# Kernel tuning notes

Measured on AMD Instinct MI355X. Metric: run time of the kernel, lower is better.

The kernel has to match this reference:

```python
import jax, jax.numpy as jnp
import numpy as np

B, N, C, K = 8, 4096, 128, 20  # batch, points-per-cloud, channels (n_cout), knn neighbors
NEG_SLOPE = 0.01  # torch F.leaky_relu default


def setup_inputs() -> dict:
    key = jax.random.key(0)
    ks = jax.random.split(key, 6)
    s = 1.0 / np.sqrt(C).astype(np.float32)
    xyz = jax.random.normal(ks[0], (B, 3, N), jnp.float32)
    points = jax.random.normal(ks[1], (B, C, N), jnp.float32)
    Wc = jax.random.normal(ks[2], (C, C), jnp.float32) * s  # center 1x1 conv weight (out,in)
    bc = jax.random.normal(ks[3], (C,), jnp.float32) * s
    Wg = jax.random.normal(ks[4], (C, C), jnp.float32) * s  # grouped 1x1 conv weight
    bg = jax.random.normal(ks[5], (C,), jnp.float32) * s
    return {"xyz": xyz, "points": points, "Wc": Wc, "bc": bc, "Wg": Wg, "bg": bg}


def reference(xyz, points, Wc, bc, Wg, bg):
    # xyz: [B,3,N], points: [B,C,N]
    k = K
    shortcut = points
    p = jax.nn.leaky_relu(points, NEG_SLOPE)        # [B,C,N]
    pt = jnp.transpose(p, (0, 2, 1))                # [B,N,C]
    xt = jnp.transpose(xyz, (0, 2, 1))              # [B,N,3]

    # pairwise squared distances [B,N,N]
    sq_norm = jnp.sum(xt * xt, axis=-1)             # [B,N]
    sq = sq_norm[:, :, None] - 2.0 * jnp.einsum('bnd,bmd->bnm', xt, xt) + sq_norm[:, None, :]

    # knn: k+1 nearest (incl. self), drop self -> [B,N,k]
    _, idx = jax.lax.top_k(-sq, k + 1)
    idx = idx[:, :, 1:]

    # gather neighbor features: [B,N,k,C]
    grouped = jax.vmap(lambda a, i: a[i])(pt, idx)

    # center 1x1 conv on [B,C,1,N] == per-point linear
    center = jnp.einsum('oc,bcn->bon', Wc, p) + bc[None, :, None]      # [B,C,N]
    # grouped 1x1 conv on [B,C,k,N]
    gout = jnp.einsum('oc,bnkc->bokn', Wg, grouped) + bg[None, :, None, None]  # [B,C,k,N]

    # mean over concat([center(1), grouped(k)], axis=2) then residual
    pooled = (center + jnp.sum(gout, axis=2)) / (k + 1)
    return pooled + shortcut
```

## Files before the change

kernel.cpp:

```cpp
#include <hip/hip_runtime.h>

#define B 8
#define N 4096
#define C 128
#define C2 256
#define KNN 21
#define CAP 22

typedef unsigned long long u64;
typedef unsigned int u32;
typedef unsigned short u16;

typedef __attribute__((ext_vector_type(8))) short bf16x8;
typedef __attribute__((ext_vector_type(4))) float f32x4;

__device__ __forceinline__ float bf2f(u16 u) {
    return __uint_as_float(((u32)u) << 16);
}
__device__ __forceinline__ u16 f2bf(float f) {
    u32 x = __float_as_uint(f);
    return (u16)((x + 0x7FFFu + ((x >> 16) & 1u)) >> 16);
}

__global__ __launch_bounds__(256) void k_transpose_lrelu(
        const float* __restrict__ pts, u16* __restrict__ X,
        const float* __restrict__ xyz, float4* __restrict__ cand) {
    __shared__ u16 tile[32][33];
    int b  = blockIdx.z;
    int c0 = blockIdx.y * 32;
    int n0 = blockIdx.x * 32;
    int tx = threadIdx.x, ty = threadIdx.y;

    if (blockIdx.y == 0 && ty == 0) {
        int n = n0 + tx;
        const float* xz = xyz + (size_t)b * 3 * N;
        float x = xz[n], y = xz[N + n], z = xz[2 * N + n];
        float sn = __fadd_rn(__fadd_rn(__fmul_rn(x, x), __fmul_rn(y, y)),
                             __fmul_rn(z, z));
        cand[(size_t)b * N + n] = make_float4(x, y, z, sn);
    }

    const float* src = pts + (size_t)b * C * N;
    #pragma unroll
    for (int i = 0; i < 32; i += 8) {
        float v = src[(size_t)(c0 + ty + i) * N + n0 + tx];
        if (v < 0.f) v = __fmul_rn(v, 0.01f);
        tile[ty + i][tx] = f2bf(v);
    }
    __syncthreads();
    u16* dst = X + (size_t)b * N * C2;
    #pragma unroll
    for (int i = 0; i < 32; i += 8) {
        dst[(size_t)(n0 + ty + i) * C2 + (c0 + tx)] = tile[tx][ty + i];
    }
}

__global__ __launch_bounds__(256) void k_knn_gather(
        const float4* __restrict__ cand, u16* __restrict__ X) {
    __shared__ __align__(16) char lds[52224];
    float4* stg  = (float4*)lds;
    u32*    kbuf = (u32*)(lds + 18432);
    u16*    ibuf = (u16*)(lds + 18432 + 22528);
    u64*    mg   = (u64*)lds;
    __shared__ u16 win[64 * KNN];

    int tid = threadIdx.x;
    int w = tid >> 6, l = tid & 63;
    int b = blockIdx.y;
    int n0 = blockIdx.x * 64;
    int nq = n0 + l;

    const float4* candb = cand + (size_t)b * N;
    float4 cq = candb[nq];
    float qx = cq.x, qy = cq.y, qz = cq.z, snq = cq.w;

    u32 key[KNN], idx[KNN];
    #pragma unroll
    for (int i = 0; i < KNN; ++i) { key[i] = 0xFFFFFFFFu; idx[i] = 0u; }
    int cnt = 0;
    u32 thr = 0xFFFFFFFFu;

    auto compact = [&]() {
        #pragma unroll 1
        for (int i = 0; i < CAP; ++i) {
            if (__ballot(i < cnt) == 0ull) break;
            u32 kv = kbuf[i * 256 + tid];
            u32 iv = ibuf[i * 256 + tid];
            bool ins = (i < cnt) && (kv < key[20]);
            if (__ballot(ins) != 0ull) {
                key[20] = ins ? kv : key[20];
                idx[20] = ins ? iv : idx[20];
                #pragma unroll
                for (int t = 19; t >= 0; --t) {
                    bool sw = key[t] > key[t + 1];
                    u32 ka = sw ? key[t + 1] : key[t];
                    u32 kz = sw ? key[t] : key[t + 1];
                    u32 ia = sw ? idx[t + 1] : idx[t];
                    u32 iz = sw ? idx[t] : idx[t + 1];
                    key[t] = ka; key[t + 1] = kz;
                    idx[t] = ia; idx[t + 1] = iz;
                }
            }
        }
        cnt = 0;
        thr = key[20];
    };

    float4* mystg = stg + w * 288;
    int wl = l + (l >> 3);

    for (int sc = 0; sc < 4; ++sc) {
        int m0 = w * 1024 + sc * 256;
        float4 v0 = candb[m0 + l];
        float4 v1 = candb[m0 + l + 64];
        float4 v2 = candb[m0 + l + 128];
        float4 v3 = candb[m0 + l + 192];
        mystg[wl]       = v0;
        mystg[wl + 72]  = v1;
        mystg[wl + 144] = v2;
        mystg[wl + 216] = v3;
        asm volatile("s_waitcnt lgkmcnt(0)" ::: "memory");
        for (int cc = 0; cc < 256; cc += 8) {
            int base = cc + (cc >> 3);
            #pragma unroll
            for (int j = 0; j < 8; ++j) {
                float4 cp = mystg[base + j];
                int m = m0 + cc + j;
                float dot = __fadd_rn(__fadd_rn(__fmul_rn(qx, cp.x),
                                                __fmul_rn(qy, cp.y)),
                                      __fmul_rn(qz, cp.z));
                float sq = __fadd_rn(__fsub_rn(snq, __fadd_rn(dot, dot)), cp.w);
                u32 bits = __float_as_uint(sq);
                u32 kb = bits ^ (0x80000000u | (u32)(((int)bits) >> 31));
                kbuf[cnt * 256 + tid] = kb;
                ibuf[cnt * 256 + tid] = (u16)m;
                cnt += (kb < thr);
            }
            if (__ballot(cnt >= 15) != 0ull) compact();
        }
    }
    compact();

    __syncthreads();
    #pragma unroll
    for (int j = 0; j < KNN; ++j)
        mg[(w * 64 + l) * KNN + j] = ((u64)key[j] << 32) | (u64)idx[j];
    __syncthreads();

    if (w == 0) {
        int p0 = 0, p1 = 0, p2 = 0, p3 = 0;
        for (int j = 0; j < KNN; ++j) {
            u64 c0 = mg[(0 * 64 + l) * KNN + p0];
            u64 c1 = mg[(1 * 64 + l) * KNN + p1];
            u64 c2 = mg[(2 * 64 + l) * KNN + p2];
            u64 c3 = mg[(3 * 64 + l) * KNN + p3];
            u64 m01 = c0 < c1 ? c0 : c1; int s01 = c0 < c1 ? 0 : 1;
            u64 m23 = c2 < c3 ? c2 : c3; int s23 = c2 < c3 ? 2 : 3;
            u64 mm = m01 < m23 ? m01 : m23;
            int sel = m01 < m23 ? s01 : s23;
            win[l * KNN + j] = (u16)(mm & 0xFFFFu);
            p0 += (sel == 0); p1 += (sel == 1); p2 += (sel == 2); p3 += (sel == 3);
        }
    }
    __syncthreads();

    const u16* Xb = X + (size_t)b * N * C2;
    for (int qq = 0; qq < 16; ++qq) {
        int q = w * 16 + qq;
        float f0 = 0.f, f1 = 0.f;
        #pragma unroll
        for (int j = 1; j < KNN; ++j) {
            int m = win[q * KNN + j];
            u32 u2 = *(const u32*)(Xb + (size_t)m * C2 + 2 * l);
            f0 += bf2f((u16)(u2 & 0xFFFFu));
            f1 += bf2f((u16)(u2 >> 16));
        }
        u16* dst = X + ((size_t)b * N + n0 + q) * C2 + 128 + 2 * l;
        *(u32*)dst = ((u32)f2bf(f1) << 16) | (u32)f2bf(f0);
    }
}

__global__ __launch_bounds__(256) void k_gemm_mfma(
        const u16* __restrict__ X, const float* __restrict__ Wc,
        const float* __restrict__ Wg, const float* __restrict__ pts,
        const float* __restrict__ bc, const float* __restrict__ bg,
        float* __restrict__ out) {
    int lb = (blockIdx.x & 7) * 128 + (blockIdx.x >> 3);
    int wid = lb * 4 + (threadIdx.x >> 6);
    int lane = threadIdx.x & 63;
    int ot = wid & 7;
    int nt = wid >> 3;
    int b  = nt >> 6;
    int n0 = (nt & 63) * 64;

    int l16 = lane & 15, lq = lane >> 4;
    const u16* Xb = X + (size_t)b * N * C2;
    const u16* bptr0 = Xb + (size_t)(n0 + 0 * 16 + l16) * C2 + lq * 8;
    const u16* bptr1 = Xb + (size_t)(n0 + 1 * 16 + l16) * C2 + lq * 8;
    const u16* bptr2 = Xb + (size_t)(n0 + 2 * 16 + l16) * C2 + lq * 8;
    const u16* bptr3 = Xb + (size_t)(n0 + 3 * 16 + l16) * C2 + lq * 8;
    const float* wrowc = Wc + (size_t)(ot * 16 + l16) * 128 + lq * 8;
    const float* wrowg = Wg + (size_t)(ot * 16 + l16) * 128 + lq * 8;

    f32x4 acc0 = {0.f, 0.f, 0.f, 0.f};
    f32x4 acc1 = {0.f, 0.f, 0.f, 0.f};
    f32x4 acc2 = {0.f, 0.f, 0.f, 0.f};
    f32x4 acc3 = {0.f, 0.f, 0.f, 0.f};
    #pragma unroll
    for (int kk = 0; kk < 8; ++kk) {
        const float* ws = (kk < 4) ? (wrowc + kk * 32) : (wrowg + (kk - 4) * 32);
        float4 wa = *(const float4*)ws;
        float4 wb = *(const float4*)(ws + 4);
        bf16x8 a;
        a[0] = (short)f2bf(wa.x); a[1] = (short)f2bf(wa.y);
        a[2] = (short)f2bf(wa.z); a[3] = (short)f2bf(wa.w);
        a[4] = (short)f2bf(wb.x); a[5] = (short)f2bf(wb.y);
        a[6] = (short)f2bf(wb.z); a[7] = (short)f2bf(wb.w);
        bf16x8 b0 = *(const bf16x8*)(bptr0 + kk * 32);
        bf16x8 b1 = *(const bf16x8*)(bptr1 + kk * 32);
        bf16x8 b2 = *(const bf16x8*)(bptr2 + kk * 32);
        bf16x8 b3 = *(const bf16x8*)(bptr3 + kk * 32);
        acc0 = __builtin_amdgcn_mfma_f32_16x16x32_bf16(a, b0, acc0, 0, 0, 0);
        acc1 = __builtin_amdgcn_mfma_f32_16x16x32_bf16(a, b1, acc1, 0, 0, 0);
        acc2 = __builtin_amdgcn_mfma_f32_16x16x32_bf16(a, b2, acc2, 0, 0, 0);
        acc3 = __builtin_amdgcn_mfma_f32_16x16x32_bf16(a, b3, acc3, 0, 0, 0);
    }

    const float inv21 = 1.0f / 21.0f;
    float bias[4];
    #pragma unroll
    for (int r = 0; r < 4; ++r) {
        int o = ot * 16 + lq * 4 + r;
        bias[r] = bc[o] + 20.f * bg[o];
    }
    const float* pb = pts + (size_t)b * C * N;
    float* ob = out + (size_t)b * C * N;
    f32x4 accs[4] = {acc0, acc1, acc2, acc3};
    #pragma unroll
    for (int t = 0; t < 4; ++t) {
        int n = n0 + t * 16 + l16;
        #pragma unroll
        for (int r = 0; r < 4; ++r) {
            int o = ot * 16 + lq * 4 + r;
            ob[(size_t)o * N + n] =
                (accs[t][r] + bias[r]) * inv21 + pb[(size_t)o * N + n];
        }
    }
}

extern "C" void kernel_launch(void* const* d_in, const int* in_sizes, int n_in,
                              void* d_out, int out_size, void* d_ws, size_t ws_size,
                              hipStream_t stream) {
    const float* xyz = (const float*)d_in[0];
    const float* pts = (const float*)d_in[1];
    const float* Wc  = (const float*)d_in[2];
    const float* bc  = (const float*)d_in[3];
    const float* Wg  = (const float*)d_in[4];
    const float* bg  = (const float*)d_in[5];
    float* out = (float*)d_out;

    u16* X = (u16*)d_ws;
    float4* cand = (float4*)((char*)d_ws +
                             (size_t)B * N * C2 * sizeof(u16));

    k_transpose_lrelu<<<dim3(N / 32, C / 32, B), dim3(32, 8), 0, stream>>>(
        pts, X, xyz, cand);
    k_knn_gather<<<dim3(N / 64, B), dim3(256), 0, stream>>>(cand, X);
    k_gemm_mfma<<<dim3(1024), dim3(256), 0, stream>>>(X, Wc, Wg, pts, bc, bg, out);
}
```

Before: 287.4 us.

## Split kNN candidate scan across eight waves per block with two-stage merge

The kNN kernel now runs 512 threads per block, so eight waves each scan 512 candidates instead of four waves scanning 1024. Per-wave partial top-21 lists are merged in two passes, first waves 0-3 into a staging list and then waves 4-7 against it, so the merge buffer fits in LDS. The buffer cap and compaction trigger are lowered to fit the larger thread count, and the padded staging layout is dropped. This shortens the serial scan per query but adds barriers, a second merge pass and more frequent compactions.

```diff
diff --git a/kernel.cpp b/kernel.cpp
--- a/kernel.cpp
+++ b/kernel.cpp
@@ -5,7 +5,7 @@
 #define C 128
 #define C2 256
 #define KNN 21
-#define CAP 22
+#define CAP 15
 
 typedef unsigned long long u64;
 typedef unsigned int u32;
@@ -55,14 +55,15 @@
     }
 }
 
-__global__ __launch_bounds__(256) void k_knn_gather(
+__global__ __launch_bounds__(512) void k_knn_gather(
         const float4* __restrict__ cand, u16* __restrict__ X) {
-    __shared__ __align__(16) char lds[52224];
+    __shared__ __align__(16) char lds[62464];
     float4* stg  = (float4*)lds;
-    u32*    kbuf = (u32*)(lds + 18432);
-    u16*    ibuf = (u16*)(lds + 18432 + 22528);
-    u64*    mg   = (u64*)lds;
-    __shared__ u16 win[64 * KNN];
+    u32*    kbuf = (u32*)(lds + 16384);
+    u16*    ibuf = (u16*)(lds + 47104);
+    u64*    mg4  = (u64*)(lds + 16384);
+    u64*    la   = (u64*)lds;
+    u16*    win  = (u16*)(lds + 10752);
 
     int tid = threadIdx.x;
     int w = tid >> 6, l = tid & 63;
@@ -84,8 +85,8 @@
         #pragma unroll 1
         for (int i = 0; i < CAP; ++i) {
             if (__ballot(i < cnt) == 0ull) break;
-            u32 kv = kbuf[i * 256 + tid];
-            u32 iv = ibuf[i * 256 + tid];
+            u32 kv = kbuf[i * 512 + tid];
+            u32 iv = ibuf[i * 512 + tid];
             bool ins = (i < cnt) && (kv < key[20]);
             if (__ballot(ins) != 0ull) {
                 key[20] = ins ? kv : key[20];
@@ -106,25 +107,19 @@
         thr = key[20];
     };
 
-    float4* mystg = stg + w * 288;
-    int wl = l + (l >> 3);
+    float4* mystg = stg + w * 128;
 
     for (int sc = 0; sc < 4; ++sc) {
-        int m0 = w * 1024 + sc * 256;
+        int m0 = w * 512 + sc * 128;
         float4 v0 = candb[m0 + l];
         float4 v1 = candb[m0 + l + 64];
-        float4 v2 = candb[m0 + l + 128];
-        float4 v3 = candb[m0 + l + 192];
-        mystg[wl]       = v0;
-        mystg[wl + 72]  = v1;
-        mystg[wl + 144] = v2;
-        mystg[wl + 216] = v3;
+        mystg[l]      = v0;
+        mystg[l + 64] = v1;
         asm volatile("s_waitcnt lgkmcnt(0)" ::: "memory");
-        for (int cc = 0; cc < 256; cc += 8) {
-            int base = cc + (cc >> 3);
+        for (int cc = 0; cc < 128; cc += 8) {
             #pragma unroll
             for (int j = 0; j < 8; ++j) {
-                float4 cp = mystg[base + j];
+                float4 cp = mystg[cc + j];
                 int m = m0 + cc + j;
                 float dot = __fadd_rn(__fadd_rn(__fmul_rn(qx, cp.x),
                                                 __fmul_rn(qy, cp.y)),
@@ -132,41 +127,74 @@
                 float sq = __fadd_rn(__fsub_rn(snq, __fadd_rn(dot, dot)), cp.w);
                 u32 bits = __float_as_uint(sq);
                 u32 kb = bits ^ (0x80000000u | (u32)(((int)bits) >> 31));
-                kbuf[cnt * 256 + tid] = kb;
-                ibuf[cnt * 256 + tid] = (u16)m;
+                kbuf[cnt * 512 + tid] = kb;
+                ibuf[cnt * 512 + tid] = (u16)m;
                 cnt += (kb < thr);
             }
-            if (__ballot(cnt >= 15) != 0ull) compact();
+            if (__ballot(cnt >= 8) != 0ull) compact();
         }
     }
     compact();
 
     __syncthreads();
-    #pragma unroll
-    for (int j = 0; j < KNN; ++j)
-        mg[(w * 64 + l) * KNN + j] = ((u64)key[j] << 32) | (u64)idx[j];
+    if (w < 4) {
+        #pragma unroll
+        for (int j = 0; j < KNN; ++j)
+            mg4[(w * 64 + l) * KNN + j] = ((u64)key[j] << 32) | (u64)idx[j];
+    }
     __syncthreads();
 
     if (w == 0) {
         int p0 = 0, p1 = 0, p2 = 0, p3 = 0;
         for (int j = 0; j < KNN; ++j) {
-            u64 c0 = mg[(0 * 64 + l) * KNN + p0];
-            u64 c1 = mg[(1 * 64 + l) * KNN + p1];
-            u64 c2 = mg[(2 * 64 + l) * KNN + p2];
-            u64 c3 = mg[(3 * 64 + l) * KNN + p3];
+            u64 c0 = mg4[(0 * 64 + l) * KNN + p0];
+            u64 c1 = mg4[(1 * 64 + l) * KNN + p1];
+            u64 c2 = mg4[(2 * 64 + l) * KNN + p2];
+            u64 c3 = mg4[(3 * 64 + l) * KNN + p3];
             u64 m01 = c0 < c1 ? c0 : c1; int s01 = c0 < c1 ? 0 : 1;
             u64 m23 = c2 < c3 ? c2 : c3; int s23 = c2 < c3 ? 2 : 3;
             u64 mm = m01 < m23 ? m01 : m23;
             int sel = m01 < m23 ? s01 : s23;
+            la[l * KNN + j] = mm;
+            p0 += (sel == 0); p1 += (sel == 1); p2 += (sel == 2); p3 += (sel == 3);
+        }
+    }
+    __syncthreads();
+
+    if (w >= 4) {
+        #pragma unroll
+        for (int j = 0; j < KNN; ++j)
+            mg4[((w - 4) * 64 + l) * KNN + j] = ((u64)key[j] << 32) | (u64)idx[j];
+    }
+    __syncthreads();
+
+    if (w == 0) {
+        int p0 = 0, p1 = 0, p2 = 0, p3 = 0, pa = 0;
+        for (int j = 0; j < KNN; ++j) {
+            u64 c0 = mg4[(0 * 64 + l) * KNN + p0];
+            u64 c1 = mg4[(1 * 64 + l) * KNN + p1];
+            u64 c2 = mg4[(2 * 64 + l) * KNN + p2];
+            u64 c3 = mg4[(3 * 64 + l) * KNN + p3];
+            u64 ca = la[l * KNN + pa];
+            u64 m01 = c0 < c1 ? c0 : c1; int s01 = c0 < c1 ? 0 : 1;
+            u64 m23 = c2 < c3 ? c2 : c3; int s23 = c2 < c3 ? 2 : 3;
+            u64 mA = m01 < m23 ? m01 : m23;
+            int sel = m01 < m23 ? s01 : s23;
+            bool useA = ca < mA;
+            u64 mm = useA ? ca : mA;
             win[l * KNN + j] = (u16)(mm & 0xFFFFu);
-            p0 += (sel == 0); p1 += (sel == 1); p2 += (sel == 2); p3 += (sel == 3);
+            pa += useA;
+            if (!useA) {
+                p0 += (sel == 0); p1 += (sel == 1);
+                p2 += (sel == 2); p3 += (sel == 3);
+            }
         }
     }
     __syncthreads();
 
     const u16* Xb = X + (size_t)b * N * C2;
-    for (int qq = 0; qq < 16; ++qq) {
-        int q = w * 16 + qq;
+    for (int qq = 0; qq < 8; ++qq) {
+        int q = w * 8 + qq;
         float f0 = 0.f, f1 = 0.f;
         #pragma unroll
         for (int j = 1; j < KNN; ++j) {
@@ -265,6 +293,6 @@
 
     k_transpose_lrelu<<<dim3(N / 32, C / 32, B), dim3(32, 8), 0, stream>>>(
         pts, X, xyz, cand);
-    k_knn_gather<<<dim3(N / 64, B), dim3(256), 0, stream>>>(cand, X);
+    k_knn_gather<<<dim3(N / 64, B), dim3(512), 0, stream>>>(cand, X);
     k_gemm_mfma<<<dim3(1024), dim3(256), 0, stream>>>(X, Wc, Wg, pts, bc, bg, out);
 }
```

New measurement: 312.9 us. 1.09x slower.

## Share per-wave kNN thresholds across waves to prune candidate insertions

Applied to the files above, without the earlier changes.

Each of the four waves scans a different quarter of the candidates for the same 64 queries. Each wave now publishes its current 21st-best distance to LDS. Every wave then rejects candidates worse than the tightest threshold published by the other waves, since those cannot reach the global top-21. This is meant to cut buffer fills and the costly sorted-insertion compaction passes. It costs three volatile LDS reads per 8 candidates and tolerates stale thresholds. Keys are now kept as raw floats, and the sortable-uint conversion moves to the final merge.

```diff
diff --git a/kernel.cpp b/kernel.cpp
--- a/kernel.cpp
+++ b/kernel.cpp
@@ -63,6 +63,7 @@
     u16*    ibuf = (u16*)(lds + 18432 + 22528);
     u64*    mg   = (u64*)lds;
     __shared__ u16 win[64 * KNN];
+    __shared__ float sthr[4][64];
 
     int tid = threadIdx.x;
     int w = tid >> 6, l = tid & 63;
@@ -74,17 +75,22 @@
     float4 cq = candb[nq];
     float qx = cq.x, qy = cq.y, qz = cq.z, snq = cq.w;
 
-    u32 key[KNN], idx[KNN];
-    #pragma unroll
-    for (int i = 0; i < KNN; ++i) { key[i] = 0xFFFFFFFFu; idx[i] = 0u; }
+    float key[KNN];
+    u32 idx[KNN];
+    #pragma unroll
+    for (int i = 0; i < KNN; ++i) { key[i] = __builtin_inff(); idx[i] = 0u; }
     int cnt = 0;
-    u32 thr = 0xFFFFFFFFu;
+    float thr = __builtin_inff();
+
+    sthr[w][l] = __builtin_inff();
+    __syncthreads();
+    volatile float* vsthr = &sthr[0][0];
 
     auto compact = [&]() {
         #pragma unroll 1
         for (int i = 0; i < CAP; ++i) {
             if (__ballot(i < cnt) == 0ull) break;
-            u32 kv = kbuf[i * 256 + tid];
+            float kv = __uint_as_float(kbuf[i * 256 + tid]);
             u32 iv = ibuf[i * 256 + tid];
             bool ins = (i < cnt) && (kv < key[20]);
             if (__ballot(ins) != 0ull) {
@@ -93,8 +99,8 @@
                 #pragma unroll
                 for (int t = 19; t >= 0; --t) {
                     bool sw = key[t] > key[t + 1];
-                    u32 ka = sw ? key[t + 1] : key[t];
-                    u32 kz = sw ? key[t] : key[t + 1];
+                    float ka = sw ? key[t + 1] : key[t];
+                    float kz = sw ? key[t] : key[t + 1];
                     u32 ia = sw ? idx[t + 1] : idx[t];
                     u32 iz = sw ? idx[t] : idx[t + 1];
                     key[t] = ka; key[t + 1] = kz;
@@ -104,10 +110,14 @@
         }
         cnt = 0;
         thr = key[20];
+        sthr[w][l] = key[20];
     };
 
     float4* mystg = stg + w * 288;
     int wl = l + (l >> 3);
+    int o1 = ((w + 1) & 3) * 64 + l;
+    int o2 = ((w + 2) & 3) * 64 + l;
+    int o3 = ((w + 3) & 3) * 64 + l;
 
     for (int sc = 0; sc < 4; ++sc) {
         int m0 = w * 1024 + sc * 256;
@@ -122,6 +132,7 @@
         asm volatile("s_waitcnt lgkmcnt(0)" ::: "memory");
         for (int cc = 0; cc < 256; cc += 8) {
             int base = cc + (cc >> 3);
+            float smin = fminf(fminf(vsthr[o1], vsthr[o2]), vsthr[o3]);
             #pragma unroll
             for (int j = 0; j < 8; ++j) {
                 float4 cp = mystg[base + j];
@@ -130,11 +141,9 @@
                                                 __fmul_rn(qy, cp.y)),
                                       __fmul_rn(qz, cp.z));
                 float sq = __fadd_rn(__fsub_rn(snq, __fadd_rn(dot, dot)), cp.w);
-                u32 bits = __float_as_uint(sq);
-                u32 kb = bits ^ (0x80000000u | (u32)(((int)bits) >> 31));
-                kbuf[cnt * 256 + tid] = kb;
+                kbuf[cnt * 256 + tid] = __float_as_uint(sq);
                 ibuf[cnt * 256 + tid] = (u16)m;
-                cnt += (kb < thr);
+                cnt += ((sq < thr) && (sq <= smin));
             }
             if (__ballot(cnt >= 15) != 0ull) compact();
         }
@@ -143,8 +152,11 @@
 
     __syncthreads();
     #pragma unroll
-    for (int j = 0; j < KNN; ++j)
-        mg[(w * 64 + l) * KNN + j] = ((u64)key[j] << 32) | (u64)idx[j];
+    for (int j = 0; j < KNN; ++j) {
+        u32 bits = __float_as_uint(key[j]);
+        u32 kb2 = bits ^ (0x80000000u | (u32)(((int)bits) >> 31));
+        mg[(w * 64 + l) * KNN + j] = ((u64)kb2 << 32) | (u64)idx[j];
+    }
     __syncthreads();
 
     if (w == 0) {
```

Result: slower. 337.0 us (+17.3%).
